# Kernel optimization log

Measured on AMD Instinct MI355X. Metric: run time of the kernel, lower is better.

## Reference

```python
import jax, jax.numpy as jnp
import numpy as np

B, C, H, W = 2, 256, 48, 48
NH = 4          # heads (and SE ratio)
DK = C // NH    # 64


def conv1x1(x, w, b):
    # x: [B,Cin,H,W], w: [Cout,Cin], b: [Cout]
    return jnp.einsum('oc,bchw->bohw', w, x) + b[None, :, None, None]


def rtrans(q_in, k_in, v_in, qw, qb, kw, kb, vw, vb):
    b, c, h_, w_ = q_in.shape
    n = h_ * w_
    q = conv1x1(q_in, qw, qb).reshape(b, NH, DK, n).transpose(0, 1, 3, 2)  # [B,h,N,dk]
    k = conv1x1(k_in, kw, kb).reshape(b, NH, DK, n)                         # [B,h,dk,N]
    v = conv1x1(v_in, vw, vb).reshape(b, NH, DK, n)                         # [B,h,dk,N]
    scores = jnp.einsum('bhnd,bhdm->bhnm', q, k) / jnp.sqrt(jnp.asarray(DK, q.dtype))
    attn = jax.nn.softmax(scores, axis=-1)                                  # [B,h,N,N]
    out = jnp.einsum('bhdn,bhnm->bhdm', v, attn)                            # [B,h,dk,N]
    return out.reshape(b, c, h_, w_)


def setup_inputs() -> dict:
    key = jax.random.key(0)
    ks = jax.random.split(key, 16)
    s = 0.02
    d = {
        'x': jax.random.normal(ks[0], (B, C, H, W), jnp.float32),
        'y': jax.random.normal(ks[1], (B, C, H, W), jnp.float32),
        # RScaling: fc1 Conv2d(2C, C//ratio, 1), fc2 Conv2d(C//ratio, 2C, 1); ratio=NH
        'sc_fc1_w': jax.random.normal(ks[2], (C // NH, 2 * C), jnp.float32) * s,
        'sc_fc1_b': jnp.zeros((C // NH,), jnp.float32),
        'sc_fc2_w': jax.random.normal(ks[3], (2 * C, C // NH), jnp.float32) * s,
        'sc_fc2_b': jnp.zeros((2 * C,), jnp.float32),
        # RTrans 1
        't1_qw': jax.random.normal(ks[4], (C, C), jnp.float32) * s,
        't1_qb': jnp.zeros((C,), jnp.float32),
        't1_kw': jax.random.normal(ks[5], (C, C), jnp.float32) * s,
        't1_kb': jnp.zeros((C,), jnp.float32),
        't1_vw': jax.random.normal(ks[6], (C, C), jnp.float32) * s,
        't1_vb': jnp.zeros((C,), jnp.float32),
        # RTrans 2 (ST=True)
        't2_qw': jax.random.normal(ks[7], (C, C), jnp.float32) * s,
        't2_qb': jnp.zeros((C,), jnp.float32),
        't2_kw': jax.random.normal(ks[8], (C, C), jnp.float32) * s,
        't2_kb': jnp.zeros((C,), jnp.float32),
        't2_vw': jax.random.normal(ks[9], (C, C), jnp.float32) * s,
        't2_vb': jnp.zeros((C,), jnp.float32),
        # RGating: Conv2d(2C, 2, 1)
        'gate_w': jax.random.normal(ks[10], (2, 2 * C), jnp.float32) * s,
        'gate_b': jnp.zeros((2,), jnp.float32),
    }
    return d


def reference(x, y, sc_fc1_w, sc_fc1_b, sc_fc2_w, sc_fc2_b,
              t1_qw, t1_qb, t1_kw, t1_kb, t1_vw, t1_vb,
              t2_qw, t2_qb, t2_kw, t2_kb, t2_vw, t2_vb,
              gate_w, gate_b):
    c = x.shape[1]
    # --- RScaling (SE squeeze-excite on concatenated streams) ---
    cat = jnp.concatenate([x, y], axis=1)                       # [B,2C,H,W]
    pooled = cat.mean(axis=(2, 3), keepdims=True)               # [B,2C,1,1]
    f = conv1x1(jax.nn.relu(conv1x1(pooled, sc_fc1_w, sc_fc1_b)), sc_fc2_w, sc_fc2_b)
    g = jax.nn.sigmoid(f)                                       # [B,2C,1,1]
    x = x * g[:, :c] + x
    y = y * g[:, c:] + y
    # --- RTrans 1: x = attn(q=x, k=y, v=y) ---
    x = rtrans(x, y, y, t1_qw, t1_qb, t1_kw, t1_kb, t1_vw, t1_vb)
    # --- RTrans 2 (ST): y = attn(q=y, k=x_new, v=x_new) ---
    y = rtrans(y, x, x, t2_qw, t2_qb, t2_kw, t2_kb, t2_vw, t2_vb)
    # --- RGating ---
    gate = jax.nn.sigmoid(conv1x1(jnp.concatenate([x, y], axis=1), gate_w, gate_b))  # [B,2,H,W]
    x = x * gate[:, :1] + x
    y = y * gate[:, 1:] + y
    return (x, y)
```

## Files before the change

kernel.cpp:

```cpp
#include <hip/hip_runtime.h>
#include <hip/hip_bf16.h>
#include <math.h>

typedef __hip_bfloat16 bf16;
typedef unsigned short u16;
typedef __attribute__((ext_vector_type(8))) short short8;
typedef __attribute__((ext_vector_type(4))) float f32x4;

#define BB  2
#define CC  256
#define NHH 4
#define DKK 64
#define NN  2304
#define NT  36
#define NT2 18
#define MS  4
#define NTM 9
#define WSTR 72
#define MFMA16(a,b,c) __builtin_amdgcn_mfma_f32_16x16x32_bf16(a, b, c, 0, 0, 0)

__device__ __forceinline__ float u2f(u16 u){ return __uint_as_float(((unsigned)u) << 16); }
__device__ __forceinline__ u16 f2u(float f){
    unsigned u = __float_as_uint(f);
    unsigned r = u + 0x7FFFu + ((u >> 16) & 1u);
    return (u16)(r >> 16);
}

__device__ __forceinline__ float ldv(const void* p, size_t i, int bf){
    return bf ? u2f(((const u16*)p)[i]) : ((const float*)p)[i];
}
__device__ __forceinline__ void stv(void* p, size_t i, float v, int bf){
    if (bf) ((u16*)p)[i] = f2u(v);
    else    ((float*)p)[i] = v;
}
__device__ __forceinline__ short8 ldw8(const void* p, size_t i, int bf){
    if (bf) return *(const short8*)((const u16*)p + i);
    const float* f = (const float*)p + i;
    short8 r;
    #pragma unroll
    for (int k = 0; k < 8; k++) r[k] = (short)f2u(f[k]);
    return r;
}

__global__ void pool_kernel(const void* __restrict__ x, const void* __restrict__ y,
                            int* __restrict__ flg, float* __restrict__ pooled){
    int t = threadIdx.x;
    const u16* u = (const u16*)x;
    bool ok = true;
    if (t < 64){
        #pragma unroll
        for (int i = 0; i < 8; i++){
            u16 v = u[t*8 + i];
            int e = (v >> 7) & 0xFF;
            ok = ok && (((v & 0x7FFF) == 0) || (e >= 96 && e <= 143));
        }
    }
    unsigned long long bl = __ballot(ok);
    __shared__ int bfs;
    if (t == 0) bfs = (bl == 0xFFFFFFFFFFFFFFFFull) ? 1 : 0;
    __syncthreads();
    int bf = bfs;
    if (blockIdx.x == 0 && t == 0) *flg = bf;

    int bid = blockIdx.x;
    int b = bid >> 9, cc = bid & 511;
    const void* src = (cc < CC) ? x : y;
    size_t base = ((size_t)b*CC + (cc & 255))*NN;
    float s = 0.f;
    for (int i = t; i < NN; i += 256) s += ldv(src, base + i, bf);
    __shared__ float red[4];
    for (int off = 32; off; off >>= 1) s += __shfl_down(s, off, 64);
    if ((t & 63) == 0) red[t >> 6] = s;
    __syncthreads();
    if (t == 0)
        pooled[bid] = (red[0]+red[1]+red[2]+red[3]) * (1.0f/(float)NN);
}

__launch_bounds__(512)
__global__ void se_kernel(const float* __restrict__ pooled,
                          const void* __restrict__ w1, const void* __restrict__ b1,
                          const void* __restrict__ w2, const void* __restrict__ b2v,
                          const int* __restrict__ flg, float* __restrict__ gse){
    int bf = *flg;
    int b = blockIdx.x;
    int t = threadIdx.x;
    __shared__ float ps[512];
    __shared__ float r1[64][9];
    __shared__ float f1s[64];
    ps[t] = pooled[b*512 + t];
    __syncthreads();
    int f = t >> 3, sub = t & 7;
    float a = 0.f;
    for (int i = 0; i < 64; i++){
        int c = sub*64 + i;
        a += ldv(w1, (size_t)f*512 + c, bf) * ps[c];
    }
    r1[f][sub] = a;
    __syncthreads();
    if (t < 64){
        float s = ldv(b1, t, bf);
        #pragma unroll
        for (int k = 0; k < 8; k++) s += r1[t][k];
        f1s[t] = fmaxf(s, 0.f);
    }
    __syncthreads();
    float a2 = ldv(b2v, t, bf);
    #pragma unroll
    for (int j = 0; j < 64; j++) a2 += ldv(w2, (size_t)t*64 + j, bf) * f1s[j];
    gse[b*512 + t] = 1.f + 1.f/(1.f + __expf(-a2));
}

__global__ void transpose2_kernel(const void* __restrict__ x, const void* __restrict__ y,
                                  const float* __restrict__ gse, const int* __restrict__ flg,
                                  u16* __restrict__ xsT, u16* __restrict__ ysT){
    int bf = *flg;
    int z = blockIdx.z;
    int b = z >> 1, which = z & 1;
    const void* src = which ? y : x;
    const float* gs = gse + b*512 + (which ? 256 : 0);
    u16* dst = which ? ysT : xsT;
    int ct = blockIdx.y, nt = blockIdx.x;
    int t = threadIdx.x;
    int nl = t & 63, cq = t >> 6;
    #pragma unroll
    for (int i = 0; i < 16; i++){
        int c = ct*64 + cq*16 + i;
        float v = ldv(src, ((size_t)b*CC + c)*NN + nt*64 + nl, bf) * gs[c];
        dst[((size_t)b*NN + nt*64 + nl)*CC + c] = f2u(v);
    }
}

__launch_bounds__(256)
__global__ void conv3_mfma(const u16* __restrict__ Xq, const u16* __restrict__ Xkv,
                           const void* __restrict__ wq, const void* __restrict__ bq,
                           const void* __restrict__ wk, const void* __restrict__ bk,
                           const void* __restrict__ wv, const void* __restrict__ bv_,
                           const int* __restrict__ flg,
                           u16* __restrict__ QT, u16* __restrict__ KT, u16* __restrict__ Vb){
    int bf = *flg;
    int bhD = blockIdx.x & 7;
    int q = blockIdx.x >> 3;
    int op = q / 36, nt = q % 36;
    int b = bhD >> 2, ot = bhD & 3;
    const u16* X = (op == 0) ? Xq : Xkv;
    const void* W    = (op == 0) ? wq : (op == 1) ? wk : wv;
    const void* bias = (op == 0) ? bq : (op == 1) ? bk : bv_;
    u16* Y = (op == 0) ? QT : (op == 1) ? KT : Vb;
    int transT = (op < 2);
    float oscale = (op == 1) ? 0.125f : 1.0f;
    int lane = threadIdx.x & 63, wv_ = threadIdx.x >> 6;
    int c15 = lane & 15, quad = lane >> 4;
    const u16* Xb = X + ((size_t)b*NN + nt*64)*CC;
    int oa = ot*64 + wv_*16 + c15;
    f32x4 zf = {0.f,0.f,0.f,0.f};
    f32x4 acc[4] = {zf,zf,zf,zf};
    #pragma unroll
    for (int kc = 0; kc < CC; kc += 32){
        short8 aw = ldw8(W, (size_t)oa*CC + kc + quad*8, bf);
        #pragma unroll
        for (int j = 0; j < 4; j++){
            short8 bx = *(const short8*)(Xb + (size_t)(j*16 + c15)*CC + kc + quad*8);
            acc[j] = MFMA16(aw, bx, acc[j]);
        }
    }
    int od = ot*64 + wv_*16 + quad*4;
    float bvr[4];
    #pragma unroll
    for (int r = 0; r < 4; r++) bvr[r] = ldv(bias, od + r, bf);
    #pragma unroll
    for (int j = 0; j < 4; j++){
        int n = nt*64 + j*16 + c15;
        #pragma unroll
        for (int r = 0; r < 4; r++){
            int o = od + r;
            float val = (acc[j][r] + bvr[r]) * oscale;
            size_t idx = transT
              ? (((size_t)(b*NHH + (o >> 6))*NN + n)*DKK + (o & 63))
              : (((size_t)b*CC + o)*NN + n);
            Y[idx] = f2u(val);
        }
    }
}

__launch_bounds__(256)
__global__ void attn_stats_mfma(const u16* __restrict__ QT, const u16* __restrict__ KT,
                                float* __restrict__ gL){
    int bh = blockIdx.x & 7;
    int r2 = blockIdx.x >> 3;
    int ntile = r2 % 36, ms = r2 / 36;
    int lane = threadIdx.x & 63, wv = threadIdx.x >> 6;
    int c15 = lane & 15, quad = lane >> 4;
    const u16* Qb = QT + (size_t)bh*NN*DKK;
    const u16* Kb = KT + (size_t)bh*NN*DKK;
    size_t qo = (size_t)(ntile*64 + wv*16 + c15)*DKK + quad*8;
    short8 a0 = *(const short8*)(Qb + qo);
    short8 a1 = *(const short8*)(Qb + qo + 32);
    float ll[4] = {0.f,0.f,0.f,0.f};
    f32x4 z = {0.f,0.f,0.f,0.f};
    for (int it = 0; it < NTM; it++){
        int mt = ms*NTM + it;
        f32x4 s[4];
        #pragma unroll
        for (int j = 0; j < 4; j++){
            size_t ko = (size_t)(mt*64 + j*16 + c15)*DKK + quad*8;
            short8 b0 = *(const short8*)(Kb + ko);
            short8 b1 = *(const short8*)(Kb + ko + 32);
            f32x4 t = MFMA16(a0, b0, z);
            s[j]     = MFMA16(a1, b1, t);
        }
        #pragma unroll
        for (int r = 0; r < 4; r++)
            ll[r] += __expf(s[0][r]) + __expf(s[1][r]) + __expf(s[2][r]) + __expf(s[3][r]);
    }
    #pragma unroll
    for (int d = 1; d < 16; d <<= 1)
        #pragma unroll
        for (int r = 0; r < 4; r++)
            ll[r] += __shfl_xor(ll[r], d, 16);
    if (c15 == 0){
        #pragma unroll
        for (int r = 0; r < 4; r++){
            int n = ntile*64 + wv*16 + quad*4 + r;
            gL[((size_t)ms*BB*NHH + bh)*NN + n] = ll[r];
        }
    }
}

__launch_bounds__(512)
__global__ void attn_out_mfma(const u16* __restrict__ QT, const u16* __restrict__ KT,
                              const u16* __restrict__ V, const float* __restrict__ gL,
                              const int* __restrict__ flg,
                              void* __restrict__ O, size_t ooff, u16* __restrict__ OT){
    int bf = *flg;
    int bh = blockIdx.x & 7;
    int mtile = blockIdx.x >> 3;
    int tid = threadIdx.x;
    int lane = tid & 63, wv5 = tid >> 6;
    int g = wv5 >> 2, wv = wv5 & 3;
    int c15 = lane & 15, quad = lane >> 4;
    const u16* Qb = QT + (size_t)bh*NN*DKK;
    const u16* Kb = KT + (size_t)bh*NN*DKK;
    const u16* Vb = V + (size_t)bh*DKK*NN;
    __shared__ __align__(16) u16 wT[2][2][64][WSTR];
    __shared__ __align__(16) float osum[64][66];
    __shared__ __align__(16) float Lis[NN];

    const size_t BHN = (size_t)BB*NHH*NN;
    for (int i = tid; i < NN; i += 512){
        size_t o = (size_t)bh*NN + i;
        Lis[i] = 1.f / (gL[o] + gL[BHN + o] + gL[2*BHN + o] + gL[3*BHN + o]);
    }
    __syncthreads();

    short8 kb0[4], kb1[4];
    #pragma unroll
    for (int j = 0; j < 4; j++){
        size_t ko = (size_t)(mtile*64 + j*16 + c15)*DKK + quad*8;
        kb0[j] = *(const short8*)(Kb + ko);
        kb1[j] = *(const short8*)(Kb + ko + 32);
    }
    f32x4 z = {0.f,0.f,0.f,0.f};
    f32x4 o4[4] = {z,z,z,z};
    int nt0 = g*NT2;
    size_t qo0 = (size_t)(nt0*64 + wv*16 + c15)*DKK + quad*8;
    short8 a0 = *(const short8*)(Qb + qo0);
    short8 a1 = *(const short8*)(Qb + qo0 + 32);
    size_t vo0 = (size_t)(wv*16 + c15)*NN + nt0*64 + quad*8;
    short8 av0 = *(const short8*)(Vb + vo0);
    short8 av1 = *(const short8*)(Vb + vo0 + 32);
    for (int it = 0; it < NT2; it++){
        int nt = g*NT2 + it;
        int p = it & 1;
        f32x4 s[4];
        #pragma unroll
        for (int j = 0; j < 4; j++){
            f32x4 t = MFMA16(a0, kb0[j], z);
            s[j]    = MFMA16(a1, kb1[j], t);
        }
        short8 a0n = a0, a1n = a1, av0n = av0, av1n = av1;
        if (it + 1 < NT2){
            size_t qn = (size_t)((nt+1)*64 + wv*16 + c15)*DKK + quad*8;
            a0n = *(const short8*)(Qb + qn);
            a1n = *(const short8*)(Qb + qn + 32);
            size_t vn = (size_t)(wv*16 + c15)*NN + (nt+1)*64 + quad*8;
            av0n = *(const short8*)(Vb + vn);
            av1n = *(const short8*)(Vb + vn + 32);
        }
        int nb = nt*64 + wv*16 + quad*4;
        float iL[4];
        #pragma unroll
        for (int r = 0; r < 4; r++) iL[r] = Lis[nb+r];
        #pragma unroll
        for (int j = 0; j < 4; j++){
            ushort4 pk;
            pk.x = f2u(__expf(s[j][0]) * iL[0]);
            pk.y = f2u(__expf(s[j][1]) * iL[1]);
            pk.z = f2u(__expf(s[j][2]) * iL[2]);
            pk.w = f2u(__expf(s[j][3]) * iL[3]);
            *(ushort4*)&wT[g][p][j*16 + c15][wv*16 + quad*4] = pk;
        }
        __syncthreads();
        #pragma unroll
        for (int j = 0; j < 4; j++){
            short8 b0 = *(const short8*)&wT[g][p][j*16 + c15][quad*8];
            short8 b1 = *(const short8*)&wT[g][p][j*16 + c15][32 + quad*8];
            o4[j] = MFMA16(av0, b0, o4[j]);
            o4[j] = MFMA16(av1, b1, o4[j]);
        }
        a0 = a0n; a1 = a1n; av0 = av0n; av1 = av1n;
    }
    if (g == 1){
        #pragma unroll
        for (int j = 0; j < 4; j++)
            #pragma unroll
            for (int r = 0; r < 4; r++)
                osum[wv*16 + quad*4 + r][j*16 + c15] = o4[j][r];
    }
    __syncthreads();
    if (g == 0){
        int brow = bh >> 2, head = bh & 3;
        #pragma unroll
        for (int j = 0; j < 4; j++){
            int m = mtile*64 + j*16 + c15;
            #pragma unroll
            for (int r = 0; r < 4; r++){
                int d = wv*16 + quad*4 + r;
                float val = o4[j][r] + osum[d][j*16 + c15];
                stv(O, ooff + ((size_t)brow*CC + head*DKK + d)*NN + m, val, bf);
                if (OT) OT[((size_t)brow*NN + m)*CC + head*DKK + d] = f2u(val);
            }
        }
    }
}

__global__ void gate_part_kernel(const void* __restrict__ out, const void* __restrict__ gw,
                                 const int* __restrict__ flg, float* __restrict__ gpart){
    int bf = *flg;
    const size_t SZ = (size_t)BB*CC*NN;
    int b = blockIdx.z, g = blockIdx.y;
    int nb = blockIdx.x*64;
    int t = threadIdx.x;
    int nl = t & 63, sub = t >> 6;
    __shared__ float r0[4][64], r1[4][64];
    float a0 = 0.f, a1 = 0.f;
    int cbase = g*128 + sub*32;
    for (int i = 0; i < 32; i++){
        int cc = cbase + i;
        size_t idx = (cc < 256 ? ((size_t)b*CC + cc)*NN
                               : SZ + ((size_t)b*CC + (cc-256))*NN) + nb + nl;
        float v = ldv(out, idx, bf);
        a0 += ldv(gw, cc, bf)*v;
        a1 += ldv(gw, 512 + cc, bf)*v;
    }
    r0[sub][nl] = a0; r1[sub][nl] = a1;
    __syncthreads();
    if (t < 64){
        float s0 = r0[0][t]+r0[1][t]+r0[2][t]+r0[3][t];
        float s1 = r1[0][t]+r1[1][t]+r1[2][t]+r1[3][t];
        int n = nb + t;
        gpart[(((size_t)b*4 + g)*2 + 0)*NN + n] = s0;
        gpart[(((size_t)b*4 + g)*2 + 1)*NN + n] = s1;
    }
}

__global__ void rescale_gates_kernel(const float* __restrict__ gpart, const void* __restrict__ gb,
                                     const int* __restrict__ flg, void* __restrict__ out){
    int bf = *flg;
    const size_t SZ = (size_t)BB*CC*NN;
    int nt = blockIdx.x, cgrp = blockIdx.y, b = blockIdx.z;
    int t = threadIdx.x;
    int j = (cgrp >= 4) ? 1 : 0;
    __shared__ float gsh[64];
    if (t < 64){
        int n = nt*64 + t;
        float s = ldv(gb, j, bf);
        #pragma unroll
        for (int g = 0; g < 4; g++)
            s += gpart[(((size_t)b*4 + g)*2 + j)*NN + n];
        gsh[t] = 1.f + 1.f/(1.f + __expf(-s));
    }
    __syncthreads();
    int nl = t & 63, cq = t >> 6;
    int cbase = (cgrp & 3)*64;
    size_t base = j ? SZ : 0;
    float gv = gsh[nl];
    #pragma unroll
    for (int i = 0; i < 16; i++){
        int c = cbase + cq*16 + i;
        size_t idx = base + ((size_t)b*CC + c)*NN + nt*64 + nl;
        stv(out, idx, ldv(out, idx, bf) * gv, bf);
    }
}

extern "C" void kernel_launch(void* const* d_in, const int* in_sizes, int n_in,
                              void* d_out, int out_size, void* d_ws, size_t ws_size,
                              hipStream_t stream){
    (void)in_sizes; (void)n_in; (void)out_size; (void)ws_size;
    const void* x    = d_in[0];
    const void* y    = d_in[1];
    const void* sc1w = d_in[2];
    const void* sc1b = d_in[3];
    const void* sc2w = d_in[4];
    const void* sc2b = d_in[5];
    const void *t1qw = d_in[6],  *t1qb = d_in[7];
    const void *t1kw = d_in[8],  *t1kb = d_in[9];
    const void *t1vw = d_in[10], *t1vb = d_in[11];
    const void *t2qw = d_in[12], *t2qb = d_in[13];
    const void *t2kw = d_in[14], *t2kb = d_in[15];
    const void *t2vw = d_in[16], *t2vb = d_in[17];
    const void *gw   = d_in[18], *gb   = d_in[19];

    const size_t SZ = (size_t)BB*CC*NN;
    const size_t BHN = (size_t)BB*NHH*NN;
    char* wsb = (char*)d_ws;
    int*   flg    = (int*)wsb;
    float* pooled = (float*)(wsb + 16);
    float* gse    = pooled + 1024;
    float* gL     = gse + 1024;
    float* gpart  = gL + MS*BHN;
    u16* xsT = (u16*)(gpart + (size_t)BB*4*2*NN);
    u16* ysT = xsT + SZ;
    u16* QT  = ysT + SZ;
    u16* KT  = QT + SZ;
    u16* Vb  = KT + SZ;

    dim3 tg2(NT, 4, BB*2);
    dim3 gg(NT, 4, BB);
    dim3 rg(NT, 8, BB);

    pool_kernel<<<1024, 256, 0, stream>>>(x, y, flg, pooled);
    se_kernel<<<BB, 512, 0, stream>>>(pooled, sc1w, sc1b, sc2w, sc2b, flg, gse);
    transpose2_kernel<<<tg2, 256, 0, stream>>>(x, y, gse, flg, xsT, ysT);

    conv3_mfma<<<864, 256, 0, stream>>>(xsT, ysT, t1qw, t1qb, t1kw, t1kb, t1vw, t1vb,
                                        flg, QT, KT, Vb);
    attn_stats_mfma<<<1152, 256, 0, stream>>>(QT, KT, gL);
    attn_out_mfma<<<288, 512, 0, stream>>>(QT, KT, Vb, gL, flg, d_out, 0, xsT);

    conv3_mfma<<<864, 256, 0, stream>>>(ysT, xsT, t2qw, t2qb, t2kw, t2kb, t2vw, t2vb,
                                        flg, QT, KT, Vb);
    attn_stats_mfma<<<1152, 256, 0, stream>>>(QT, KT, gL);
    attn_out_mfma<<<288, 512, 0, stream>>>(QT, KT, Vb, gL, flg, d_out, SZ, (u16*)nullptr);

    gate_part_kernel<<<gg, 256, 0, stream>>>(d_out, gw, flg, gpart);
    rescale_gates_kernel<<<rg, 256, 0, stream>>>(gpart, gb, flg, d_out);
}
```

Baseline: 402.7 us.

## Software-pipeline QK scores one tile ahead and use exp2 with prescaled K

After: 408.1 us. Within noise of the previous version (+1.3%).

```diff
diff --git a/kernel.cpp b/kernel.cpp
--- a/kernel.cpp
+++ b/kernel.cpp
@@ -17,6 +17,7 @@
 #define MS  4
 #define NTM 9
 #define WSTR 72
+#define KSCALE 0.18033688011f
 #define MFMA16(a,b,c) __builtin_amdgcn_mfma_f32_16x16x32_bf16(a, b, c, 0, 0, 0)
 
 __device__ __forceinline__ float u2f(u16 u){ return __uint_as_float(((unsigned)u) << 16); }
@@ -147,7 +148,7 @@
     const void* bias = (op == 0) ? bq : (op == 1) ? bk : bv_;
     u16* Y = (op == 0) ? QT : (op == 1) ? KT : Vb;
     int transT = (op < 2);
-    float oscale = (op == 1) ? 0.125f : 1.0f;
+    float oscale = (op == 1) ? KSCALE : 1.0f;
     int lane = threadIdx.x & 63, wv_ = threadIdx.x >> 6;
     int c15 = lane & 15, quad = lane >> 4;
     const u16* Xb = X + ((size_t)b*NN + nt*64)*CC;
@@ -210,7 +211,7 @@
         }
         #pragma unroll
         for (int r = 0; r < 4; r++)
-            ll[r] += __expf(s[0][r]) + __expf(s[1][r]) + __expf(s[2][r]) + __expf(s[3][r]);
+            ll[r] += exp2f(s[0][r]) + exp2f(s[1][r]) + exp2f(s[2][r]) + exp2f(s[3][r]);
     }
     #pragma unroll
     for (int d = 1; d < 16; d <<= 1)
@@ -261,53 +262,78 @@
     }
     f32x4 z = {0.f,0.f,0.f,0.f};
     f32x4 o4[4] = {z,z,z,z};
-    int nt0 = g*NT2;
-    size_t qo0 = (size_t)(nt0*64 + wv*16 + c15)*DKK + quad*8;
-    short8 a0 = *(const short8*)(Qb + qo0);
-    short8 a1 = *(const short8*)(Qb + qo0 + 32);
-    size_t vo0 = (size_t)(wv*16 + c15)*NN + nt0*64 + quad*8;
-    short8 av0 = *(const short8*)(Vb + vo0);
-    short8 av1 = *(const short8*)(Vb + vo0 + 32);
+
+    int base = g*NT2;
+    short8 qn0, qn1, vc0, vc1, vn0, vn1;
+    {
+        size_t qo = (size_t)((base+0)*64 + wv*16 + c15)*DKK + quad*8;
+        short8 qc0 = *(const short8*)(Qb + qo);
+        short8 qc1 = *(const short8*)(Qb + qo + 32);
+        size_t vo = (size_t)(wv*16 + c15)*NN + (base+0)*64 + quad*8;
+        vc0 = *(const short8*)(Vb + vo);
+        vc1 = *(const short8*)(Vb + vo + 32);
+        size_t qo1 = (size_t)((base+1)*64 + wv*16 + c15)*DKK + quad*8;
+        qn0 = *(const short8*)(Qb + qo1);
+        qn1 = *(const short8*)(Qb + qo1 + 32);
+        size_t vo1 = (size_t)(wv*16 + c15)*NN + (base+1)*64 + quad*8;
+        vn0 = *(const short8*)(Vb + vo1);
+        vn1 = *(const short8*)(Vb + vo1 + 32);
+    }
+    f32x4 sc[4];
+    {
+        size_t qo = (size_t)((base+0)*64 + wv*16 + c15)*DKK + quad*8;
+        short8 qc0 = *(const short8*)(Qb + qo);
+        short8 qc1 = *(const short8*)(Qb + qo + 32);
+        #pragma unroll
+        for (int j = 0; j < 4; j++){
+            f32x4 t = MFMA16(qc0, kb0[j], z);
+            sc[j]   = MFMA16(qc1, kb1[j], t);
+        }
+    }
+
     for (int it = 0; it < NT2; it++){
-        int nt = g*NT2 + it;
+        int nt = base + it;
         int p = it & 1;
-        f32x4 s[4];
-        #pragma unroll
-        for (int j = 0; j < 4; j++){
-            f32x4 t = MFMA16(a0, kb0[j], z);
-            s[j]    = MFMA16(a1, kb1[j], t);
-        }
-        short8 a0n = a0, a1n = a1, av0n = av0, av1n = av1;
+        int nb = nt*64 + wv*16 + quad*4;
+        float iL0 = Lis[nb], iL1 = Lis[nb+1], iL2 = Lis[nb+2], iL3 = Lis[nb+3];
+        #pragma unroll
+        for (int j = 0; j < 4; j++){
+            __hip_bfloat162 h01 = __float22bfloat162_rn(
+                make_float2(exp2f(sc[j][0])*iL0, exp2f(sc[j][1])*iL1));
+            __hip_bfloat162 h23 = __float22bfloat162_rn(
+                make_float2(exp2f(sc[j][2])*iL2, exp2f(sc[j][3])*iL3));
+            uint2 pk = make_uint2(*(unsigned*)&h01, *(unsigned*)&h23);
+            *(uint2*)&wT[g][p][j*16 + c15][wv*16 + quad*4] = pk;
+        }
+        f32x4 sn[4];
         if (it + 1 < NT2){
-            size_t qn = (size_t)((nt+1)*64 + wv*16 + c15)*DKK + quad*8;
-            a0n = *(const short8*)(Qb + qn);
-            a1n = *(const short8*)(Qb + qn + 32);
-            size_t vn = (size_t)(wv*16 + c15)*NN + (nt+1)*64 + quad*8;
-            av0n = *(const short8*)(Vb + vn);
-            av1n = *(const short8*)(Vb + vn + 32);
-        }
-        int nb = nt*64 + wv*16 + quad*4;
-        float iL[4];
-        #pragma unroll
-        for (int r = 0; r < 4; r++) iL[r] = Lis[nb+r];
-        #pragma unroll
-        for (int j = 0; j < 4; j++){
-            ushort4 pk;
-            pk.x = f2u(__expf(s[j][0]) * iL[0]);
-            pk.y = f2u(__expf(s[j][1]) * iL[1]);
-            pk.z = f2u(__expf(s[j][2]) * iL[2]);
-            pk.w = f2u(__expf(s[j][3]) * iL[3]);
-            *(ushort4*)&wT[g][p][j*16 + c15][wv*16 + quad*4] = pk;
+            #pragma unroll
+            for (int j = 0; j < 4; j++){
+                f32x4 t = MFMA16(qn0, kb0[j], z);
+                sn[j]   = MFMA16(qn1, kb1[j], t);
+            }
+        }
+        if (it + 2 < NT2){
+            size_t qo = (size_t)((nt+2)*64 + wv*16 + c15)*DKK + quad*8;
+            qn0 = *(const short8*)(Qb + qo);
+            qn1 = *(const short8*)(Qb + qo + 32);
         }
         __syncthreads();
         #pragma unroll
         for (int j = 0; j < 4; j++){
             short8 b0 = *(const short8*)&wT[g][p][j*16 + c15][quad*8];
             short8 b1 = *(const short8*)&wT[g][p][j*16 + c15][32 + quad*8];
-            o4[j] = MFMA16(av0, b0, o4[j]);
-            o4[j] = MFMA16(av1, b1, o4[j]);
-        }
-        a0 = a0n; a1 = a1n; av0 = av0n; av1 = av1n;
+            o4[j] = MFMA16(vc0, b0, o4[j]);
+            o4[j] = MFMA16(vc1, b1, o4[j]);
+        }
+        vc0 = vn0; vc1 = vn1;
+        if (it + 2 < NT2){
+            size_t vo = (size_t)(wv*16 + c15)*NN + (nt+2)*64 + quad*8;
+            vn0 = *(const short8*)(Vb + vo);
+            vn1 = *(const short8*)(Vb + vo + 32);
+        }
+        #pragma unroll
+        for (int j = 0; j < 4; j++) sc[j] = sn[j];
     }
     if (g == 1){
         #pragma unroll
```
